# Performance work log

Hardware: AMD Instinct MI355X
Metric: run time of the kernel (lower is better)

The kernel has to match this reference:

```python
import jax, jax.numpy as jnp
import numpy as np

B, TQ, TKV, D, H = 4, 1024, 1024, 1024, 16
HD = D // H  # head_size = 64
EPS = 1e-5


def setup_inputs() -> dict:
    key = jax.random.key(0)
    ks = jax.random.split(key, 5)
    s = 0.02
    return {
        "x_q": jax.random.normal(ks[0], (B, TQ, D), jnp.float32),
        "x_kv": jax.random.normal(ks[1], (B, TKV, D), jnp.float32),
        "Wq": jax.random.normal(ks[2], (D, 2 * D), jnp.float32) * s,
        "Wkv": jax.random.normal(ks[3], (D, 3 * D), jnp.float32) * s,
        "Wc": jax.random.normal(ks[4], (D, D), jnp.float32) * s,
        "qn1": jnp.ones((HD,), jnp.float32),
        "kn1": jnp.ones((HD,), jnp.float32),
        "qn2": jnp.ones((HD,), jnp.float32),
        "kn2": jnp.ones((HD,), jnp.float32),
        "gn_w": jnp.ones((D,), jnp.float32),
        "gn_b": jnp.zeros((D,), jnp.float32),
        "lmb": jnp.full((1, H, 1, 1), -4.0, jnp.float32),
    }


def _rms(x, w):
    # RMSNorm over last dim (head_size), eps=1e-5, learned scale w
    return x * jax.lax.rsqrt(jnp.mean(x * x, axis=-1, keepdims=True) + EPS) * w


def _heads(t, T):
    # (B,T,D) -> (B,H,T,HD)
    return t.reshape(B, T, H, HD).transpose(0, 2, 1, 3)


def _attn(q, k, v):
    att = jnp.einsum('bhqd,bhkd->bhqk', q, k) * (1.0 / np.sqrt(HD))
    att = jax.nn.softmax(att, axis=-1)
    return jnp.einsum('bhqk,bhkd->bhqd', att, v)


def reference(x_q, x_kv, Wq, Wkv, Wc, qn1, kn1, qn2, kn2, gn_w, gn_b, lmb):
    q1, q2 = jnp.split(x_q @ Wq, 2, axis=-1)
    k1, k2, v = jnp.split(x_kv @ Wkv, 3, axis=-1)
    q1 = _rms(_heads(q1, TQ), qn1)
    q2 = _rms(_heads(q2, TQ), qn2)
    k1 = _rms(_heads(k1, TKV), kn1)
    k2 = _rms(_heads(k2, TKV), kn2)
    v = _heads(v, TKV)
    y = _attn(q1, k1, v) - jax.nn.softplus(lmb) * _attn(q2, k2, v)  # (B,H,TQ,HD)
    # GroupNorm(n_head groups over n_embd channels), input (B,C,TQ):
    # per (batch, head) stats over (TQ, HD)
    mu = jnp.mean(y, axis=(2, 3), keepdims=True)
    var = jnp.var(y, axis=(2, 3), keepdims=True)
    yn = (y - mu) * jax.lax.rsqrt(var + EPS)
    yn = yn * gn_w.reshape(1, H, 1, HD) + gn_b.reshape(1, H, 1, HD)
    y = yn.transpose(0, 2, 1, 3).reshape(B, TQ, D)
    return y @ Wc
```

## Files before the change

kernel.cpp:

```cpp
#include <hip/hip_runtime.h>
#include <cstdint>
#include <cstddef>

#define B_ 4
#define TQ_ 1024
#define TKV_ 1024
#define D_ 1024
#define H_ 16
#define HD_ 64

typedef __bf16 bf16_t;
typedef bf16_t bf16x4 __attribute__((ext_vector_type(4)));
typedef bf16_t bf16x8 __attribute__((ext_vector_type(8)));
typedef float f32x4 __attribute__((ext_vector_type(4)));

#if __has_builtin(__builtin_amdgcn_exp2f)
#define EXP2F __builtin_amdgcn_exp2f
#else
#define EXP2F exp2f
#endif

__device__ __forceinline__ bf16_t to_bf16(float f) {
  uint32_t u = __builtin_bit_cast(uint32_t, f);
  u += 0x7fffu + ((u >> 16) & 1u);
  uint16_t h = (uint16_t)(u >> 16);
  return __builtin_bit_cast(bf16_t, h);
}
__device__ __forceinline__ float bf2f(bf16_t b) {
  uint32_t u = ((uint32_t)__builtin_bit_cast(uint16_t, b)) << 16;
  return __builtin_bit_cast(float, u);
}
__device__ __forceinline__ uint32_t pack_bf16_trunc(float lo, float hi) {
  return __builtin_amdgcn_perm(__builtin_bit_cast(uint32_t, hi),
                               __builtin_bit_cast(uint32_t, lo), 0x07060302u);
}
__device__ __forceinline__ void gload_lds16(const void* g, void* l) {
  __builtin_amdgcn_global_load_lds((const __attribute__((address_space(1))) void*)g,
                                   (__attribute__((address_space(3))) void*)l, 16, 0, 0);
}

__global__ __launch_bounds__(256) void k_f2b2(const float* __restrict__ xq,
                                              const float* __restrict__ xkv,
                                              bf16_t* __restrict__ oq,
                                              bf16_t* __restrict__ okv) {
  int blk = blockIdx.x;
  const float* in = (blk < 4096) ? xq : xkv;
  bf16_t* out = (blk < 4096) ? oq : okv;
  int i = (blk & 4095) * 256 + threadIdx.x;
  float4 v = ((const float4*)in)[i];
  bf16x4 o = {to_bf16(v.x), to_bf16(v.y), to_bf16(v.z), to_bf16(v.w)};
  *(bf16x4*)(out + (size_t)i * 4) = o;
}

__global__ __launch_bounds__(256) void k_trb3(const float* __restrict__ Wq,
                                              const float* __restrict__ Wkv,
                                              const float* __restrict__ Wc,
                                              bf16_t* __restrict__ Wqt,
                                              bf16_t* __restrict__ Wkvt,
                                              bf16_t* __restrict__ Wct) {
  __shared__ float tile[32][33];
  int x = blockIdx.x;
  const float* in;
  bf16_t* out;
  int C, c0;
  if (x < 64) { in = Wq; out = Wqt; C = 2048; c0 = x * 32; }
  else if (x < 160) { in = Wkv; out = Wkvt; C = 3072; c0 = (x - 64) * 32; }
  else { in = Wc; out = Wct; C = 1024; c0 = (x - 160) * 32; }
  int r0 = blockIdx.y * 32;
  int tx = threadIdx.x & 31, ty = threadIdx.x >> 5;
#pragma unroll
  for (int i = 0; i < 4; i++)
    tile[ty + i * 8][tx] = in[(size_t)(r0 + ty + i * 8) * C + c0 + tx];
  __syncthreads();
#pragma unroll
  for (int i = 0; i < 4; i++) {
    int rr = ty + i * 8;
    out[(size_t)(c0 + rr) * 1024 + r0 + tx] = to_bf16(tile[tx][rr]);
  }
}

__global__ __launch_bounds__(256) void k_trv(const bf16_t* __restrict__ in,
                                             bf16_t* __restrict__ out) {
  __shared__ bf16_t tile[64][65];
  int bh = blockIdx.y;
  int t0 = blockIdx.x * 64;
  const bf16_t* ib = in + (size_t)bh * 65536;
  bf16_t* ob = out + (size_t)bh * 65536;
  int r = threadIdx.x >> 2, c8 = (threadIdx.x & 3) * 16;
  bf16x8 a = *(const bf16x8*)(ib + (size_t)(t0 + r) * 64 + c8);
  bf16x8 bb = *(const bf16x8*)(ib + (size_t)(t0 + r) * 64 + c8 + 8);
#pragma unroll
  for (int j = 0; j < 8; j++) {
    tile[c8 + j][r] = a[j];
    tile[c8 + 8 + j][r] = bb[j];
  }
  __syncthreads();
  int d = threadIdx.x >> 2, tt = (threadIdx.x & 3) * 16;
  bf16x8 o0, o1;
#pragma unroll
  for (int j = 0; j < 8; j++) {
    o0[j] = tile[d][tt + j];
    o1[j] = tile[d][tt + 8 + j];
  }
  *(bf16x8*)(ob + (size_t)d * 1024 + t0 + tt) = o0;
  *(bf16x8*)(ob + (size_t)d * 1024 + t0 + tt + 8) = o1;
}

__global__ __launch_bounds__(256, 2) void k_gemm_qkv(const bf16_t* __restrict__ xq,
                                                     const bf16_t* __restrict__ xkv,
                                                     const bf16_t* __restrict__ Wqt,
                                                     const bf16_t* __restrict__ Wkvt,
                                                     const float* __restrict__ kn1,
                                                     const float* __restrict__ kn2,
                                                     bf16_t* __restrict__ q12,
                                                     bf16_t* __restrict__ k1h,
                                                     bf16_t* __restrict__ k2h,
                                                     bf16_t* __restrict__ vh) {
  __shared__ bf16_t As[128 * 32];
  __shared__ bf16_t Bs[128 * 32];
  const int tid = threadIdx.x;
  const int wave = tid >> 6, lane = tid & 63;
  const int ln = lane & 15, lq = lane >> 4;
  const bool isq = blockIdx.x < 16;
  const bf16_t* A = isq ? xq : xkv;
  const bf16_t* Bt = isq ? Wqt : Wkvt;
  const int n0 = (isq ? blockIdx.x : blockIdx.x - 16) * 128;
  const int m0 = blockIdx.y * 128;
  const int wm = (wave >> 1) * 64, wn = (wave & 1) * 64;
  f32x4 acc[4][4];
#pragma unroll
  for (int i = 0; i < 4; i++)
#pragma unroll
    for (int j = 0; j < 4; j++) acc[i][j] = (f32x4){0.f, 0.f, 0.f, 0.f};

  for (int k0 = 0; k0 < 1024; k0 += 32) {
#pragma unroll
    for (int rnd = 0; rnd < 2; rnd++) {
      int c = rnd * 256 + tid;
      int row = c >> 2, col = (c & 3) * 8;
      int ldsoff = (rnd * 256 + wave * 64) * 16;
      gload_lds16(A + (size_t)(m0 + row) * 1024 + k0 + col, (char*)As + ldsoff);
      gload_lds16(Bt + (size_t)(n0 + row) * 1024 + k0 + col, (char*)Bs + ldsoff);
    }
    asm volatile("s_waitcnt vmcnt(0)" ::: "memory");
    __syncthreads();
    bf16x8 af[4], bfr[4];
#pragma unroll
    for (int i = 0; i < 4; i++) {
      af[i] = *(const bf16x8*)(As + (wm + i * 16 + ln) * 32 + lq * 8);
      bfr[i] = *(const bf16x8*)(Bs + (wn + i * 16 + ln) * 32 + lq * 8);
    }
#pragma unroll
    for (int i = 0; i < 4; i++)
#pragma unroll
      for (int j = 0; j < 4; j++)
        acc[i][j] = __builtin_amdgcn_mfma_f32_16x16x32_bf16(af[i], bfr[j], acc[i][j], 0, 0, 0);
    __syncthreads();
  }

  if (isq) {
#pragma unroll
    for (int i = 0; i < 4; i++)
#pragma unroll
      for (int j = 0; j < 4; j++)
#pragma unroll
        for (int r = 0; r < 4; r++) {
          int row = m0 + wm + i * 16 + lq * 4 + r;
          int col = n0 + wn + j * 16 + ln;
          q12[(size_t)row * 2048 + col] = to_bf16(acc[i][j][r]);
        }
  } else {
    const int col0 = n0 + wn;
    const int part = col0 >> 10;
    const int h = (col0 >> 6) & 15;
    if (part < 2) {
      const float* kn = part ? kn2 : kn1;
      bf16_t* dst = part ? k2h : k1h;
      float kw[4];
#pragma unroll
      for (int j = 0; j < 4; j++) kw[j] = kn[j * 16 + ln];
#pragma unroll
      for (int i = 0; i < 4; i++)
#pragma unroll
        for (int r = 0; r < 4; r++) {
          float ss = 0.f;
#pragma unroll
          for (int j = 0; j < 4; j++) ss += acc[i][j][r] * acc[i][j][r];
          ss += __shfl_xor(ss, 1, 64);
          ss += __shfl_xor(ss, 2, 64);
          ss += __shfl_xor(ss, 4, 64);
          ss += __shfl_xor(ss, 8, 64);
          float rstd = rsqrtf(ss * (1.f / 64.f) + 1e-5f);
          int m = m0 + wm + i * 16 + lq * 4 + r;
          int b = m >> 10, t = m & 1023;
          size_t base = (((size_t)(b * 16 + h)) * 1024 + t) * 64;
#pragma unroll
          for (int j = 0; j < 4; j++)
            dst[base + j * 16 + ln] = to_bf16(acc[i][j][r] * rstd * kw[j]);
        }
    } else {
#pragma unroll
      for (int i = 0; i < 4; i++)
#pragma unroll
        for (int r = 0; r < 4; r++) {
          int m = m0 + wm + i * 16 + lq * 4 + r;
          int b = m >> 10, t = m & 1023;
          size_t base = (((size_t)(b * 16 + h)) * 1024 + t) * 64;
#pragma unroll
          for (int j = 0; j < 4; j++)
            vh[base + j * 16 + ln] = to_bf16(acc[i][j][r]);
        }
    }
  }
}

__global__ __launch_bounds__(256, 2) void k_gemm64(const bf16_t* __restrict__ A,
                                                   const bf16_t* __restrict__ Bt,
                                                   float* __restrict__ C, int N, int K) {
  __shared__ bf16_t As[128 * 32];
  __shared__ bf16_t Bs[64 * 32];
  const int tid = threadIdx.x;
  const int wave = tid >> 6, lane = tid & 63;
  const int ln = lane & 15, lq = lane >> 4;
  const int m0 = blockIdx.y * 128, n0 = blockIdx.x * 64;
  const int wm = wave * 32;
  f32x4 acc[2][4];
#pragma unroll
  for (int i = 0; i < 2; i++)
#pragma unroll
    for (int j = 0; j < 4; j++) acc[i][j] = (f32x4){0.f, 0.f, 0.f, 0.f};

  for (int k0 = 0; k0 < K; k0 += 32) {
#pragma unroll
    for (int rnd = 0; rnd < 2; rnd++) {
      int c = rnd * 256 + tid;
      int row = c >> 2, col = (c & 3) * 8;
      int ldsoff = (rnd * 256 + wave * 64) * 16;
      gload_lds16(A + (size_t)(m0 + row) * K + k0 + col, (char*)As + ldsoff);
    }
    {
      int row = tid >> 2, col = (tid & 3) * 8;
      int ldsoff = (wave * 64) * 16;
      gload_lds16(Bt + (size_t)(n0 + row) * K + k0 + col, (char*)Bs + ldsoff);
    }
    asm volatile("s_waitcnt vmcnt(0)" ::: "memory");
    __syncthreads();
    bf16x8 af[2], bfr[4];
#pragma unroll
    for (int i = 0; i < 2; i++)
      af[i] = *(const bf16x8*)(As + (wm + i * 16 + ln) * 32 + lq * 8);
#pragma unroll
    for (int j = 0; j < 4; j++)
      bfr[j] = *(const bf16x8*)(Bs + (j * 16 + ln) * 32 + lq * 8);
#pragma unroll
    for (int i = 0; i < 2; i++)
#pragma unroll
      for (int j = 0; j < 4; j++)
        acc[i][j] = __builtin_amdgcn_mfma_f32_16x16x32_bf16(af[i], bfr[j], acc[i][j], 0, 0, 0);
    __syncthreads();
  }
#pragma unroll
  for (int i = 0; i < 2; i++)
#pragma unroll
    for (int j = 0; j < 4; j++)
#pragma unroll
      for (int r = 0; r < 4; r++) {
        int row = m0 + wm + i * 16 + lq * 4 + r;
        int col = n0 + j * 16 + ln;
        C[(size_t)row * N + col] = acc[i][j][r];
      }
}

__global__ __launch_bounds__(256, 4) void k_attn2(const bf16_t* __restrict__ q12,
                                                  const bf16_t* __restrict__ k1h,
                                                  const bf16_t* __restrict__ k2h,
                                                  const bf16_t* __restrict__ vt,
                                                  const float* __restrict__ qn1,
                                                  const float* __restrict__ qn2,
                                                  const float* __restrict__ lmb,
                                                  bf16_t* __restrict__ y) {
  __shared__ bf16_t Ks[2][4096];
  __shared__ bf16_t Vs[4096];
  const int tid = threadIdx.x;
  const int wave = tid >> 6, lane = tid & 63;
  const int ln = lane & 15, lq = lane >> 4;
  const int swz = ln & 7;
  const int bh = blockIdx.x;
  const int b = bh >> 4, h = bh & 15;
  const int q0 = blockIdx.y * 64 + wave * 16;
  const bf16_t* kb[2] = {k1h + (size_t)bh * 65536, k2h + (size_t)bh * 65536};
  const bf16_t* vb = vt + (size_t)bh * 65536;

  bf16x8 qf[2][2];
#pragma unroll
  for (int st = 0; st < 2; st++)
#pragma unroll
    for (int ks = 0; ks < 2; ks++)
      qf[st][ks] = *(const bf16x8*)(q12 + (size_t)(b * 1024 + q0 + ln) * 2048 + st * 1024 +
                                    h * 64 + ks * 32 + lq * 8);
#pragma unroll
  for (int st = 0; st < 2; st++) {
    const float* qn = st ? qn2 : qn1;
    float ssq = 0.f;
#pragma unroll
    for (int ks = 0; ks < 2; ks++)
#pragma unroll
      for (int j = 0; j < 8; j++) {
        float v = bf2f(qf[st][ks][j]);
        ssq += v * v;
      }
    ssq += __shfl_xor(ssq, 16, 64);
    ssq += __shfl_xor(ssq, 32, 64);
    float rr = rsqrtf(ssq * (1.f / 64.f) + 1e-5f) * (0.125f * 1.44269504f);
#pragma unroll
    for (int ks = 0; ks < 2; ks++)
#pragma unroll
      for (int j = 0; j < 8; j++)
        qf[st][ks][j] = to_bf16(bf2f(qf[st][ks][j]) * rr * qn[ks * 32 + lq * 8 + j]);
  }

  f32x4 O[2][4];
  float lp[2] = {0.f, 0.f};
#pragma unroll
  for (int st = 0; st < 2; st++)
#pragma unroll
    for (int nt = 0; nt < 4; nt++) O[st][nt] = (f32x4){0.f, 0.f, 0.f, 0.f};

  for (int kv0 = 0; kv0 < TKV_; kv0 += 64) {
    __syncthreads();
#pragma unroll
    for (int r = 0; r < 6; r++) {
      int a = r >> 1, r2 = r & 1;
      int g = r2 * 256 + tid;
      int row = g >> 3;
      int blk = (g & 7) ^ (row & 7);
      const bf16_t* src = (a < 2) ? (kb[a] + (size_t)(kv0 + row) * 64 + blk * 8)
                                  : (vb + (size_t)row * 1024 + kv0 + blk * 8);
      char* dst = (a < 2) ? ((char*)Ks + a * 8192) : (char*)Vs;
      gload_lds16(src, dst + (r2 * 256 + wave * 64) * 16);
    }
    asm volatile("s_waitcnt vmcnt(0)" ::: "memory");
    __syncthreads();

#pragma unroll
    for (int st = 0; st < 2; st++) {
      bf16x8 kf[2][4];
#pragma unroll
      for (int ks = 0; ks < 2; ks++)
#pragma unroll
        for (int t = 0; t < 4; t++)
          kf[ks][t] = *(const bf16x8*)(&Ks[st][((t * 16 + ln) * 8 + ((4 * ks + lq) ^ swz)) * 8]);
      f32x4 s[4];
#pragma unroll
      for (int t = 0; t < 4; t++) s[t] = (f32x4){0.f, 0.f, 0.f, 0.f};
#pragma unroll
      for (int ks = 0; ks < 2; ks++)
#pragma unroll
        for (int t = 0; t < 4; t++)
          s[t] = __builtin_amdgcn_mfma_f32_16x16x32_bf16(kf[ks][t], qf[st][ks], s[t], 0, 0, 0);
      uint32_t pfu[2][4];
      float l = 0.f;
#pragma unroll
      for (int t = 0; t < 4; t++) {
        float e0 = EXP2F(s[t][0]), e1 = EXP2F(s[t][1]);
        float e2 = EXP2F(s[t][2]), e3 = EXP2F(s[t][3]);
        l += (e0 + e1) + (e2 + e3);
        pfu[t >> 1][(t & 1) * 2] = pack_bf16_trunc(e0, e1);
        pfu[t >> 1][(t & 1) * 2 + 1] = pack_bf16_trunc(e2, e3);
      }
      lp[st] += l;
#pragma unroll
      for (int u = 0; u < 2; u++) {
        bf16x8 pf = __builtin_bit_cast(bf16x8, *(uint4*)pfu[u]);
#pragma unroll
        for (int nt = 0; nt < 4; nt++) {
          uint2 lo = *(const uint2*)(Vs + ((nt * 16 + ln) * 8 + ((u * 4 + (lq >> 1)) ^ swz)) * 8 +
                                     (lq & 1) * 4);
          uint2 hi = *(const uint2*)(Vs + ((nt * 16 + ln) * 8 + ((u * 4 + 2 + (lq >> 1)) ^ swz)) * 8 +
                                     (lq & 1) * 4);
          uint4 vq = {lo.x, lo.y, hi.x, hi.y};
          bf16x8 vfrag = __builtin_bit_cast(bf16x8, vq);
          O[st][nt] = __builtin_amdgcn_mfma_f32_16x16x32_bf16(pf, vfrag, O[st][nt], 0, 0, 0);
        }
      }
    }
  }

  float c = log1pf(__expf(lmb[h]));
  float linv[2][4];
#pragma unroll
  for (int st = 0; st < 2; st++) {
    float l = lp[st];
    l += __shfl_xor(l, 16, 64);
    l += __shfl_xor(l, 32, 64);
#pragma unroll
    for (int r = 0; r < 4; r++) linv[st][r] = 1.f / __shfl(l, lq * 4 + r, 64);
  }
#pragma unroll
  for (int nt = 0; nt < 4; nt++)
#pragma unroll
    for (int r = 0; r < 4; r++) {
      size_t a = ((size_t)bh * TQ_ + q0 + lq * 4 + r) * 64 + nt * 16 + ln;
      y[a] = to_bf16(O[0][nt][r] * linv[0][r] - c * O[1][nt][r] * linv[1][r]);
    }
}

__global__ __launch_bounds__(256) void k_gn_part(const bf16_t* __restrict__ y,
                                                 float* __restrict__ part) {
  int bh = blockIdx.x >> 2, qp = blockIdx.x & 3;
  const bf16_t* p = y + (size_t)bh * 65536 + qp * 16384;
  float s = 0.f, ss = 0.f;
  for (int i = threadIdx.x; i < 2048; i += 256) {
    bf16x8 v = *(const bf16x8*)(p + i * 8);
#pragma unroll
    for (int j = 0; j < 8; j++) {
      float f = bf2f(v[j]);
      s += f;
      ss += f * f;
    }
  }
#pragma unroll
  for (int m = 1; m < 64; m <<= 1) {
    s += __shfl_xor(s, m, 64);
    ss += __shfl_xor(ss, m, 64);
  }
  __shared__ float red[8];
  int wv = threadIdx.x >> 6;
  if ((threadIdx.x & 63) == 0) {
    red[wv] = s;
    red[4 + wv] = ss;
  }
  __syncthreads();
  if (threadIdx.x == 0) {
    part[blockIdx.x * 2] = red[0] + red[1] + red[2] + red[3];
    part[blockIdx.x * 2 + 1] = red[4] + red[5] + red[6] + red[7];
  }
}

__global__ __launch_bounds__(64) void k_gn_comb(const float* __restrict__ part,
                                                float* __restrict__ stats) {
  int bh = threadIdx.x;
  float S = 0.f, SS = 0.f;
#pragma unroll
  for (int p = 0; p < 4; p++) {
    S += part[(bh * 4 + p) * 2];
    SS += part[(bh * 4 + p) * 2 + 1];
  }
  float mean = S * (1.f / 65536.f);
  float var = SS * (1.f / 65536.f) - mean * mean;
  stats[bh * 2] = mean;
  stats[bh * 2 + 1] = rsqrtf(var + 1e-5f);
}

__global__ __launch_bounds__(256) void k_gn_apply(const bf16_t* __restrict__ y,
                                                  const float* __restrict__ stats,
                                                  const float* __restrict__ gw,
                                                  const float* __restrict__ gb,
                                                  bf16_t* __restrict__ yn) {
  int idx = blockIdx.x * 256 + threadIdx.x;
  int i = idx * 8;
  int bh = i >> 16;
  int h = bh & 15, b = bh >> 4;
  float mean = stats[bh * 2], rstd = stats[bh * 2 + 1];
  bf16x8 a = *(const bf16x8*)(y + i);
  int rem = i & 65535;
  int t = rem >> 6, d = rem & 63;
  bf16x8 o;
#pragma unroll
  for (int j = 0; j < 8; j++) {
    float f = (bf2f(a[j]) - mean) * rstd * gw[h * 64 + d + j] + gb[h * 64 + d + j];
    o[j] = to_bf16(f);
  }
  *(bf16x8*)(yn + ((size_t)(b * 1024 + t)) * 1024 + h * 64 + d) = o;
}

extern "C" void kernel_launch(void* const* d_in, const int* in_sizes, int n_in,
                              void* d_out, int out_size, void* d_ws, size_t ws_size,
                              hipStream_t stream) {
  const float* x_q = (const float*)d_in[0];
  const float* x_kv = (const float*)d_in[1];
  const float* Wq = (const float*)d_in[2];
  const float* Wkv = (const float*)d_in[3];
  const float* Wc = (const float*)d_in[4];
  const float* qn1 = (const float*)d_in[5];
  const float* kn1 = (const float*)d_in[6];
  const float* qn2 = (const float*)d_in[7];
  const float* kn2 = (const float*)d_in[8];
  const float* gn_w = (const float*)d_in[9];
  const float* gn_b = (const float*)d_in[10];
  const float* lmb = (const float*)d_in[11];

  const size_t MB = (size_t)1 << 20;
  char* ws = (char*)d_ws;
  bf16_t* xq_bf = (bf16_t*)(ws + 0 * MB);
  bf16_t* xkv_bf = (bf16_t*)(ws + 8 * MB);
  bf16_t* Wqt = (bf16_t*)(ws + 16 * MB);
  bf16_t* Wkvt = (bf16_t*)(ws + 20 * MB);
  bf16_t* Wct = (bf16_t*)(ws + 26 * MB);
  bf16_t* q12 = (bf16_t*)(ws + 28 * MB);
  bf16_t* k1h = (bf16_t*)(ws + 44 * MB);
  bf16_t* k2h = (bf16_t*)(ws + 52 * MB);
  bf16_t* vh = (bf16_t*)(ws + 60 * MB);
  bf16_t* vt = (bf16_t*)(ws + 68 * MB);
  bf16_t* y = (bf16_t*)(ws + 76 * MB);
  bf16_t* yn = (bf16_t*)(ws + 84 * MB);
  float* stats = (float*)(ws + 92 * MB);
  float* part = (float*)(ws + 92 * MB + 4096);

  k_f2b2<<<8192, 256, 0, stream>>>(x_q, x_kv, xq_bf, xkv_bf);
  k_trb3<<<dim3(192, 32), 256, 0, stream>>>(Wq, Wkv, Wc, Wqt, Wkvt, Wct);
  k_gemm_qkv<<<dim3(40, 32), 256, 0, stream>>>(xq_bf, xkv_bf, Wqt, Wkvt, kn1, kn2,
                                               q12, k1h, k2h, vh);
  k_trv<<<dim3(16, 64), 256, 0, stream>>>(vh, vt);
  k_attn2<<<dim3(64, 16), 256, 0, stream>>>(q12, k1h, k2h, vt, qn1, qn2, lmb, y);
  k_gn_part<<<256, 256, 0, stream>>>(y, part);
  k_gn_comb<<<1, 64, 0, stream>>>(part, stats);
  k_gn_apply<<<2048, 256, 0, stream>>>(y, stats, gn_w, gn_b, yn);
  k_gemm64<<<dim3(16, 32), 256, 0, stream>>>(yn, Wct, (float*)d_out, 1024, 1024);
}
```

Baseline: 270.5 us.

## Fuse prep kernels, write V transposed from GEMM, fold GroupNorm stats into attention

Merges the input bf16 conversion and weight transposes into one prep kernel, which also zeroes the GroupNorm accumulators. The QKV GEMM now writes V directly in transposed layout, so the separate V transpose kernel is gone. The attention kernel accumulates per-(batch,head) sum and sum-of-squares with atomics, which removes the gn_part and gn_comb kernels. Both GEMMs get XCD-aware block remapping for cache locality. Together this cuts launch count and memory round trips, at the cost of float atomics (nondeterministic summation order) and strided V stores.

```diff
diff --git a/kernel.cpp b/kernel.cpp
--- a/kernel.cpp
+++ b/kernel.cpp
@@ -39,71 +39,48 @@
                                    (__attribute__((address_space(3))) void*)l, 16, 0, 0);
 }
 
-__global__ __launch_bounds__(256) void k_f2b2(const float* __restrict__ xq,
+__global__ __launch_bounds__(256) void k_prep(const float* __restrict__ xq,
                                               const float* __restrict__ xkv,
-                                              bf16_t* __restrict__ oq,
-                                              bf16_t* __restrict__ okv) {
-  int blk = blockIdx.x;
-  const float* in = (blk < 4096) ? xq : xkv;
-  bf16_t* out = (blk < 4096) ? oq : okv;
-  int i = (blk & 4095) * 256 + threadIdx.x;
-  float4 v = ((const float4*)in)[i];
-  bf16x4 o = {to_bf16(v.x), to_bf16(v.y), to_bf16(v.z), to_bf16(v.w)};
-  *(bf16x4*)(out + (size_t)i * 4) = o;
-}
-
-__global__ __launch_bounds__(256) void k_trb3(const float* __restrict__ Wq,
+                                              const float* __restrict__ Wq,
                                               const float* __restrict__ Wkv,
                                               const float* __restrict__ Wc,
+                                              bf16_t* __restrict__ oq,
+                                              bf16_t* __restrict__ okv,
                                               bf16_t* __restrict__ Wqt,
                                               bf16_t* __restrict__ Wkvt,
-                                              bf16_t* __restrict__ Wct) {
-  __shared__ float tile[32][33];
-  int x = blockIdx.x;
-  const float* in;
-  bf16_t* out;
-  int C, c0;
-  if (x < 64) { in = Wq; out = Wqt; C = 2048; c0 = x * 32; }
-  else if (x < 160) { in = Wkv; out = Wkvt; C = 3072; c0 = (x - 64) * 32; }
-  else { in = Wc; out = Wct; C = 1024; c0 = (x - 160) * 32; }
-  int r0 = blockIdx.y * 32;
-  int tx = threadIdx.x & 31, ty = threadIdx.x >> 5;
-#pragma unroll
-  for (int i = 0; i < 4; i++)
-    tile[ty + i * 8][tx] = in[(size_t)(r0 + ty + i * 8) * C + c0 + tx];
-  __syncthreads();
-#pragma unroll
-  for (int i = 0; i < 4; i++) {
-    int rr = ty + i * 8;
-    out[(size_t)(c0 + rr) * 1024 + r0 + tx] = to_bf16(tile[tx][rr]);
-  }
-}
-
-__global__ __launch_bounds__(256) void k_trv(const bf16_t* __restrict__ in,
-                                             bf16_t* __restrict__ out) {
-  __shared__ bf16_t tile[64][65];
-  int bh = blockIdx.y;
-  int t0 = blockIdx.x * 64;
-  const bf16_t* ib = in + (size_t)bh * 65536;
-  bf16_t* ob = out + (size_t)bh * 65536;
-  int r = threadIdx.x >> 2, c8 = (threadIdx.x & 3) * 16;
-  bf16x8 a = *(const bf16x8*)(ib + (size_t)(t0 + r) * 64 + c8);
-  bf16x8 bb = *(const bf16x8*)(ib + (size_t)(t0 + r) * 64 + c8 + 8);
-#pragma unroll
-  for (int j = 0; j < 8; j++) {
-    tile[c8 + j][r] = a[j];
-    tile[c8 + 8 + j][r] = bb[j];
-  }
-  __syncthreads();
-  int d = threadIdx.x >> 2, tt = (threadIdx.x & 3) * 16;
-  bf16x8 o0, o1;
-#pragma unroll
-  for (int j = 0; j < 8; j++) {
-    o0[j] = tile[d][tt + j];
-    o1[j] = tile[d][tt + 8 + j];
-  }
-  *(bf16x8*)(ob + (size_t)d * 1024 + t0 + tt) = o0;
-  *(bf16x8*)(ob + (size_t)d * 1024 + t0 + tt + 8) = o1;
+                                              bf16_t* __restrict__ Wct,
+                                              float* __restrict__ part) {
+  int blk = blockIdx.x;
+  if (blk == 0 && threadIdx.x < 128) part[threadIdx.x] = 0.f;
+  if (blk < 8192) {
+    const float* in = (blk < 4096) ? xq : xkv;
+    bf16_t* out = (blk < 4096) ? oq : okv;
+    int i = (blk & 4095) * 256 + threadIdx.x;
+    float4 v = ((const float4*)in)[i];
+    bf16x4 o = {to_bf16(v.x), to_bf16(v.y), to_bf16(v.z), to_bf16(v.w)};
+    *(bf16x4*)(out + (size_t)i * 4) = o;
+  } else {
+    __shared__ float tile[32][33];
+    int t = blk - 8192;
+    int x = t % 192, yb = t / 192;
+    const float* in;
+    bf16_t* out;
+    int C, c0;
+    if (x < 64) { in = Wq; out = Wqt; C = 2048; c0 = x * 32; }
+    else if (x < 160) { in = Wkv; out = Wkvt; C = 3072; c0 = (x - 64) * 32; }
+    else { in = Wc; out = Wct; C = 1024; c0 = (x - 160) * 32; }
+    int r0 = yb * 32;
+    int tx = threadIdx.x & 31, ty = threadIdx.x >> 5;
+#pragma unroll
+    for (int i = 0; i < 4; i++)
+      tile[ty + i * 8][tx] = in[(size_t)(r0 + ty + i * 8) * C + c0 + tx];
+    __syncthreads();
+#pragma unroll
+    for (int i = 0; i < 4; i++) {
+      int rr = ty + i * 8;
+      out[(size_t)(c0 + rr) * 1024 + r0 + tx] = to_bf16(tile[tx][rr]);
+    }
+  }
 }
 
 __global__ __launch_bounds__(256, 2) void k_gemm_qkv(const bf16_t* __restrict__ xq,
@@ -115,17 +92,30 @@
                                                      bf16_t* __restrict__ q12,
                                                      bf16_t* __restrict__ k1h,
                                                      bf16_t* __restrict__ k2h,
-                                                     bf16_t* __restrict__ vh) {
+                                                     bf16_t* __restrict__ vt) {
   __shared__ bf16_t As[128 * 32];
   __shared__ bf16_t Bs[128 * 32];
   const int tid = threadIdx.x;
   const int wave = tid >> 6, lane = tid & 63;
   const int ln = lane & 15, lq = lane >> 4;
-  const bool isq = blockIdx.x < 16;
+
+  const int fid = blockIdx.x;
+  const int xcd = fid & 7, l = fid >> 3;
+  bool isq;
+  int xb, yb;
+  if (l < 64) {
+    isq = true;
+    xb = (xcd & 3) * 4 + (l & 3);
+    yb = (xcd >> 2) * 16 + (l >> 2);
+  } else {
+    isq = false;
+    int l2 = l - 64;
+    xb = (xcd & 3) * 6 + l2 % 6;
+    yb = (xcd >> 2) * 16 + l2 / 6;
+  }
   const bf16_t* A = isq ? xq : xkv;
   const bf16_t* Bt = isq ? Wqt : Wkvt;
-  const int n0 = (isq ? blockIdx.x : blockIdx.x - 16) * 128;
-  const int m0 = blockIdx.y * 128;
+  const int n0 = xb * 128, m0 = yb * 128;
   const int wm = (wave >> 1) * 64, wn = (wave & 1) * 64;
   f32x4 acc[4][4];
 #pragma unroll
@@ -171,11 +161,13 @@
         }
   } else {
     const int col0 = n0 + wn;
-    const int part = col0 >> 10;
+    const int part3 = col0 >> 10;
     const int h = (col0 >> 6) & 15;
-    if (part < 2) {
-      const float* kn = part ? kn2 : kn1;
-      bf16_t* dst = part ? k2h : k1h;
+    const int b = m0 >> 10;
+    const int bh = b * 16 + h;
+    if (part3 < 2) {
+      const float* kn = part3 ? kn2 : kn1;
+      bf16_t* dst = part3 ? k2h : k1h;
       float kw[4];
 #pragma unroll
       for (int j = 0; j < 4; j++) kw[j] = kn[j * 16 + ln];
@@ -192,24 +184,25 @@
           ss += __shfl_xor(ss, 8, 64);
           float rstd = rsqrtf(ss * (1.f / 64.f) + 1e-5f);
           int m = m0 + wm + i * 16 + lq * 4 + r;
-          int b = m >> 10, t = m & 1023;
-          size_t base = (((size_t)(b * 16 + h)) * 1024 + t) * 64;
+          int t = m & 1023;
+          size_t base = ((size_t)bh * 1024 + t) * 64;
 #pragma unroll
           for (int j = 0; j < 4; j++)
             dst[base + j * 16 + ln] = to_bf16(acc[i][j][r] * rstd * kw[j]);
         }
     } else {
-#pragma unroll
-      for (int i = 0; i < 4; i++)
-#pragma unroll
-        for (int r = 0; r < 4; r++) {
-          int m = m0 + wm + i * 16 + lq * 4 + r;
-          int b = m >> 10, t = m & 1023;
-          size_t base = (((size_t)(b * 16 + h)) * 1024 + t) * 64;
-#pragma unroll
-          for (int j = 0; j < 4; j++)
-            vh[base + j * 16 + ln] = to_bf16(acc[i][j][r]);
+      bf16_t* obase = vt + (size_t)bh * 65536;
+#pragma unroll
+      for (int i = 0; i < 4; i++) {
+        int t0 = (m0 & 1023) + wm + i * 16 + lq * 4;
+#pragma unroll
+        for (int j = 0; j < 4; j++) {
+          bf16x4 pv;
+#pragma unroll
+          for (int r = 0; r < 4; r++) pv[r] = to_bf16(acc[i][j][r]);
+          *(bf16x4*)(obase + (size_t)(j * 16 + ln) * 1024 + t0) = pv;
         }
+      }
     }
   }
 }
@@ -222,7 +215,11 @@
   const int tid = threadIdx.x;
   const int wave = tid >> 6, lane = tid & 63;
   const int ln = lane & 15, lq = lane >> 4;
-  const int m0 = blockIdx.y * 128, n0 = blockIdx.x * 64;
+  const int fid = blockIdx.x;
+  const int xcd = fid & 7, l = fid >> 3;
+  const int lx = l & 1, ly = (l >> 1) & 15, yh = l >> 5;
+  const int n0 = (xcd * 2 + lx) * 64;
+  const int m0 = (yh * 16 + ly) * 128;
   const int wm = wave * 32;
   f32x4 acc[2][4];
 #pragma unroll
@@ -278,7 +275,8 @@
                                                   const float* __restrict__ qn1,
                                                   const float* __restrict__ qn2,
                                                   const float* __restrict__ lmb,
-                                                  bf16_t* __restrict__ y) {
+                                                  bf16_t* __restrict__ y,
+                                                  float* __restrict__ part) {
   __shared__ bf16_t Ks[2][4096];
   __shared__ bf16_t Vs[4096];
   const int tid = threadIdx.x;
@@ -396,64 +394,30 @@
 #pragma unroll
     for (int r = 0; r < 4; r++) linv[st][r] = 1.f / __shfl(l, lq * 4 + r, 64);
   }
+  float s_acc = 0.f, ss_acc = 0.f;
 #pragma unroll
   for (int nt = 0; nt < 4; nt++)
 #pragma unroll
     for (int r = 0; r < 4; r++) {
       size_t a = ((size_t)bh * TQ_ + q0 + lq * 4 + r) * 64 + nt * 16 + ln;
-      y[a] = to_bf16(O[0][nt][r] * linv[0][r] - c * O[1][nt][r] * linv[1][r]);
-    }
-}
-
-__global__ __launch_bounds__(256) void k_gn_part(const bf16_t* __restrict__ y,
-                                                 float* __restrict__ part) {
-  int bh = blockIdx.x >> 2, qp = blockIdx.x & 3;
-  const bf16_t* p = y + (size_t)bh * 65536 + qp * 16384;
-  float s = 0.f, ss = 0.f;
-  for (int i = threadIdx.x; i < 2048; i += 256) {
-    bf16x8 v = *(const bf16x8*)(p + i * 8);
-#pragma unroll
-    for (int j = 0; j < 8; j++) {
-      float f = bf2f(v[j]);
-      s += f;
-      ss += f * f;
-    }
-  }
+      float val = O[0][nt][r] * linv[0][r] - c * O[1][nt][r] * linv[1][r];
+      s_acc += val;
+      ss_acc += val * val;
+      y[a] = to_bf16(val);
+    }
 #pragma unroll
   for (int m = 1; m < 64; m <<= 1) {
-    s += __shfl_xor(s, m, 64);
-    ss += __shfl_xor(ss, m, 64);
-  }
-  __shared__ float red[8];
-  int wv = threadIdx.x >> 6;
-  if ((threadIdx.x & 63) == 0) {
-    red[wv] = s;
-    red[4 + wv] = ss;
-  }
-  __syncthreads();
-  if (threadIdx.x == 0) {
-    part[blockIdx.x * 2] = red[0] + red[1] + red[2] + red[3];
-    part[blockIdx.x * 2 + 1] = red[4] + red[5] + red[6] + red[7];
-  }
-}
-
-__global__ __launch_bounds__(64) void k_gn_comb(const float* __restrict__ part,
-                                                float* __restrict__ stats) {
-  int bh = threadIdx.x;
-  float S = 0.f, SS = 0.f;
-#pragma unroll
-  for (int p = 0; p < 4; p++) {
-    S += part[(bh * 4 + p) * 2];
-    SS += part[(bh * 4 + p) * 2 + 1];
-  }
-  float mean = S * (1.f / 65536.f);
-  float var = SS * (1.f / 65536.f) - mean * mean;
-  stats[bh * 2] = mean;
-  stats[bh * 2 + 1] = rsqrtf(var + 1e-5f);
+    s_acc += __shfl_xor(s_acc, m, 64);
+    ss_acc += __shfl_xor(ss_acc, m, 64);
+  }
+  if (lane == 0) {
+    atomicAdd(&part[bh * 2], s_acc);
+    atomicAdd(&part[bh * 2 + 1], ss_acc);
+  }
 }
 
 __global__ __launch_bounds__(256) void k_gn_apply(const bf16_t* __restrict__ y,
-                                                  const float* __restrict__ stats,
+                                                  const float* __restrict__ part,
                                                   const float* __restrict__ gw,
                                                   const float* __restrict__ gb,
                                                   bf16_t* __restrict__ yn) {
@@ -461,7 +425,10 @@
   int i = idx * 8;
   int bh = i >> 16;
   int h = bh & 15, b = bh >> 4;
-  float mean = stats[bh * 2], rstd = stats[bh * 2 + 1];
+  float S = part[bh * 2], SS = part[bh * 2 + 1];
+  float mean = S * (1.f / 65536.f);
+  float var = SS * (1.f / 65536.f) - mean * mean;
+  float rstd = rsqrtf(var + 1e-5f);
   bf16x8 a = *(const bf16x8*)(y + i);
   int rem = i & 65535;
   int t = rem >> 6, d = rem & 63;
@@ -500,21 +467,16 @@
   bf16_t* q12 = (bf16_t*)(ws + 28 * MB);
   bf16_t* k1h = (bf16_t*)(ws + 44 * MB);
   bf16_t* k2h = (bf16_t*)(ws + 52 * MB);
-  bf16_t* vh = (bf16_t*)(ws + 60 * MB);
-  bf16_t* vt = (bf16_t*)(ws + 68 * MB);
-  bf16_t* y = (bf16_t*)(ws + 76 * MB);
-  bf16_t* yn = (bf16_t*)(ws + 84 * MB);
-  float* stats = (float*)(ws + 92 * MB);
-  float* part = (float*)(ws + 92 * MB + 4096);
-
-  k_f2b2<<<8192, 256, 0, stream>>>(x_q, x_kv, xq_bf, xkv_bf);
-  k_trb3<<<dim3(192, 32), 256, 0, stream>>>(Wq, Wkv, Wc, Wqt, Wkvt, Wct);
-  k_gemm_qkv<<<dim3(40, 32), 256, 0, stream>>>(xq_bf, xkv_bf, Wqt, Wkvt, kn1, kn2,
-                                               q12, k1h, k2h, vh);
-  k_trv<<<dim3(16, 64), 256, 0, stream>>>(vh, vt);
-  k_attn2<<<dim3(64, 16), 256, 0, stream>>>(q12, k1h, k2h, vt, qn1, qn2, lmb, y);
-  k_gn_part<<<256, 256, 0, stream>>>(y, part);
-  k_gn_comb<<<1, 64, 0, stream>>>(part, stats);
-  k_gn_apply<<<2048, 256, 0, stream>>>(y, stats, gn_w, gn_b, yn);
-  k_gemm64<<<dim3(16, 32), 256, 0, stream>>>(yn, Wct, (float*)d_out, 1024, 1024);
-}
+  bf16_t* vt = (bf16_t*)(ws + 60 * MB);
+  bf16_t* y = (bf16_t*)(ws + 68 * MB);
+  bf16_t* yn = (bf16_t*)(ws + 76 * MB);
+  float* part = (float*)(ws + 84 * MB);
+
+  k_prep<<<14336, 256, 0, stream>>>(x_q, x_kv, Wq, Wkv, Wc, xq_bf, xkv_bf, Wqt, Wkvt, Wct,
+                                    part);
+  k_gemm_qkv<<<1280, 256, 0, stream>>>(xq_bf, xkv_bf, Wqt, Wkvt, kn1, kn2, q12, k1h, k2h,
+                                       vt);
+  k_attn2<<<dim3(64, 16), 256, 0, stream>>>(q12, k1h, k2h, vt, qn1, qn2, lmb, y, part);
+  k_gn_apply<<<2048, 256, 0, stream>>>(y, part, gn_w, gn_b, yn);
+  k_gemm64<<<512, 256, 0, stream>>>(yn, Wct, (float*)d_out, 1024, 1024);
+}
```

Result: no change. 268.6 us (-0.7%).
